# Kernel optimization log

Measured on AMD Instinct MI355X. Metric: run time of the kernel, lower is better.

## Reference

```python
import jax, jax.numpy as jnp
import numpy as np

MARGIN = 0.2
EPS = 1e-6


def setup_inputs() -> dict:
    key = jax.random.key(0)
    k1, k2 = jax.random.split(key)
    B, C = 8192, 1024
    z_label = jax.random.randint(k1, (B,), 0, 256, dtype=jnp.int64 if jax.config.jax_enable_x64 else jnp.int32)
    z_idx = jnp.arange(B, dtype=z_label.dtype)
    z = jax.random.normal(k2, (B, C), dtype=jnp.float32)
    return {"z_label": z_label, "z_idx": z_idx, "z": z}


def reference(z_label, z_idx, z):
    B = z.shape[0]
    k = max(2, int(B * 0.01))  # static: labels overwritten if batch has a single unique label
    all_same = jnp.all(z_label == z_label[0])
    z_label = jnp.where(all_same & (jnp.arange(B) < k), -1, z_label)

    # Vectorized triplet mining (replaces per-sample Python loop):
    # positive: first j with same label, different sample idx; negative: first j with different label.
    label_eq = z_label[:, None] == z_label[None, :]            # [B, B]
    pos_mask = label_eq & (z_idx[:, None] != z_idx[None, :])   # [B, B]
    neg_mask = ~label_eq                                       # [B, B]
    pos_idx = jnp.argmax(pos_mask, axis=1)  # first True (torch.where(...)[0][0])
    neg_idx = jnp.argmax(neg_mask, axis=1)
    valid = pos_mask.any(axis=1) & neg_mask.any(axis=1)        # [B]

    # TripletMarginLoss (p=2, swap=False): d(x,y) = ||x - y + eps||_2
    a, p_emb, n_emb = z, z[pos_idx], z[neg_idx]
    d_ap = jnp.sqrt(jnp.sum((a - p_emb + EPS) ** 2, axis=1))
    d_an = jnp.sqrt(jnp.sum((a - n_emb + EPS) ** 2, axis=1))
    per = jnp.maximum(d_ap - d_an + MARGIN, 0.0)               # [B]

    n_valid = valid.sum()
    vf = valid.astype(per.dtype)
    loss = jnp.where(n_valid > 0,
                     jnp.sum(per * vf) / jnp.maximum(n_valid, 1).astype(per.dtype),
                     jnp.array(0.0, per.dtype))
    return loss
```

## Files before the change

kernel.cpp:

```cpp
#include <hip/hip_runtime.h>

#define MARGIN 0.2f
#define EPSC 1e-6f
#define INF_I 0x7fffffff

__global__ __launch_bounds__(1024) void mine_kernel(
    const int* __restrict__ label, const int* __restrict__ zidx, int B,
    int* __restrict__ g_pos, int* __restrict__ g_neg, int* __restrict__ g_valid)
{
    __shared__ int s_label[8192];
    __shared__ int s_first[258];
    __shared__ int s_second[258];
    __shared__ int s_fd_orig;
    __shared__ int s_fd_eff;
    const int tid = threadIdx.x;
    const int T   = blockDim.x;

    if (tid < 258) { s_first[tid] = INF_I; s_second[tid] = INF_I; }
    if (tid == 0) { s_fd_orig = INF_I; s_fd_eff = INF_I; }
    if ((B & 3) == 0) {
        for (int j = tid * 4; j < B; j += T * 4) {
            int4 v = *(const int4*)(label + j);
            s_label[j] = v.x; s_label[j+1] = v.y; s_label[j+2] = v.z; s_label[j+3] = v.w;
        }
    } else {
        for (int j = tid; j < B; j += T) s_label[j] = label[j];
    }
    __syncthreads();

    const int l0 = s_label[0];
    int lm = INF_I;
    for (int j = tid; j < B; j += T) { if (s_label[j] != l0) { lm = j; break; } }
    if (lm != INF_I) atomicMin(&s_fd_orig, lm);
    __syncthreads();

    const bool all_same = (s_fd_orig == INF_I);
    int k = B / 100; if (k < 2) k = 2;
    if (all_same) { for (int j = tid; j < k && j < B; j += T) s_label[j] = -1; }
    __syncthreads();

    const int l0e = s_label[0];
    lm = INF_I;
    for (int j = tid; j < B; j += T) {
        int l = s_label[j];
        atomicMin(&s_first[l + 1], j);
        if (l != l0e && j < lm) lm = j;
    }
    if (lm != INF_I) atomicMin(&s_fd_eff, lm);
    __syncthreads();

    for (int j = tid; j < B; j += T) {
        int l = s_label[j];
        if (j != s_first[l + 1]) atomicMin(&s_second[l + 1], j);
    }
    __syncthreads();

    const int fd = s_fd_eff;
    for (int i = tid; i < B; i += T) {
        int l  = s_label[i];
        int fo = s_first[l + 1];
        int myidx = zidx[i];
        int pos; bool vp;
        if (zidx[fo] != myidx) { pos = fo; vp = true; }
        else {
            int so = s_second[l + 1];
            if (so != INF_I) { pos = so; vp = true; }
            else             { pos = 0;  vp = false; }
        }
        int neg; bool vn;
        if (l != l0e)        { neg = 0;  vn = true; }
        else if (fd != INF_I){ neg = fd; vn = true; }
        else                 { neg = 0;  vn = false; }
        g_pos[i] = pos; g_neg[i] = neg; g_valid[i] = (vp && vn) ? 1 : 0;
    }
}

__device__ inline void acc8(const float4& av, const float4& pv, const float4& nv,
                            float& sap, float& san) {
    float d;
    d = av.x - pv.x + EPSC; sap += d * d;
    d = av.y - pv.y + EPSC; sap += d * d;
    d = av.z - pv.z + EPSC; sap += d * d;
    d = av.w - pv.w + EPSC; sap += d * d;
    d = av.x - nv.x + EPSC; san += d * d;
    d = av.y - nv.y + EPSC; san += d * d;
    d = av.z - nv.z + EPSC; san += d * d;
    d = av.w - nv.w + EPSC; san += d * d;
}

__global__ __launch_bounds__(256) void dist_kernel(
    const float* __restrict__ z, const int* __restrict__ g_pos,
    const int* __restrict__ g_neg, const int* __restrict__ g_valid,
    int B, int C, float* __restrict__ g_bsum, float* __restrict__ g_bcnt)
{
    const int wave = threadIdx.x >> 6;
    const int lane = threadIdx.x & 63;
    const int i = blockIdx.x * 4 + wave;

    float lsum = 0.f, lcnt = 0.f;
    if (i < B) {
        const float4* a = (const float4*)(z + (size_t)i * C) + lane;
        const float4* p = (const float4*)(z + (size_t)g_pos[i] * C) + lane;
        const float4* n = (const float4*)(z + (size_t)g_neg[i] * C) + lane;
        float sap = 0.f, san = 0.f;
        if (C == 1024) {
            float4 a0 = a[0], a1 = a[64], a2 = a[128], a3 = a[192];
            float4 p0 = p[0], p1 = p[64], p2 = p[128], p3 = p[192];
            float4 n0 = n[0], n1 = n[64], n2 = n[128], n3 = n[192];
            acc8(a0, p0, n0, sap, san);
            acc8(a1, p1, n1, sap, san);
            acc8(a2, p2, n2, sap, san);
            acc8(a3, p3, n3, sap, san);
        } else {
            const int nk = C >> 8;
            for (int k = 0; k < nk; ++k)
                acc8(a[k * 64], p[k * 64], n[k * 64], sap, san);
            for (int c = (nk << 8) + lane; c < C; c += 64) {
                float av = z[(size_t)i * C + c];
                float pv = z[(size_t)g_pos[i] * C + c];
                float nv = z[(size_t)g_neg[i] * C + c];
                float d = av - pv + EPSC; sap += d * d;
                d = av - nv + EPSC; san += d * d;
            }
        }
        for (int off = 32; off; off >>= 1) {
            sap += __shfl_xor(sap, off, 64);
            san += __shfl_xor(san, off, 64);
        }
        if (lane == 0 && g_valid[i]) {
            lsum = fmaxf(sqrtf(sap) - sqrtf(san) + MARGIN, 0.f);
            lcnt = 1.f;
        }
    }

    __shared__ float s_sum[4], s_cnt[4];
    if (lane == 0) { s_sum[wave] = lsum; s_cnt[wave] = lcnt; }
    __syncthreads();
    if (threadIdx.x == 0) {
        float bs = 0.f, bc = 0.f;
        for (int w = 0; w < 4; ++w) { bs += s_sum[w]; bc += s_cnt[w]; }
        g_bsum[blockIdx.x] = bs;
        g_bcnt[blockIdx.x] = bc;
    }
}

__global__ __launch_bounds__(256) void final_kernel(
    const float* __restrict__ g_bsum, const float* __restrict__ g_bcnt,
    int nb, float* __restrict__ out)
{
    const int t = threadIdx.x;
    float s = 0.f, c = 0.f;
    for (int i = t; i < nb; i += blockDim.x) { s += g_bsum[i]; c += g_bcnt[i]; }
    for (int off = 32; off; off >>= 1) {
        s += __shfl_xor(s, off, 64);
        c += __shfl_xor(c, off, 64);
    }
    __shared__ float s_s[4], s_c[4];
    const int wave = t >> 6, lane = t & 63;
    if (lane == 0) { s_s[wave] = s; s_c[wave] = c; }
    __syncthreads();
    if (t == 0) {
        float ts = 0.f, tc = 0.f;
        for (int w = 0; w < 4; ++w) { ts += s_s[w]; tc += s_c[w]; }
        out[0] = (tc > 0.f) ? ts / tc : 0.f;
    }
}

extern "C" void kernel_launch(void* const* d_in, const int* in_sizes, int n_in,
                              void* d_out, int out_size, void* d_ws, size_t ws_size,
                              hipStream_t stream) {
    const int*   z_label = (const int*)d_in[0];
    const int*   z_idx   = (const int*)d_in[1];
    const float* z       = (const float*)d_in[2];
    const int B = in_sizes[0];
    const int C = in_sizes[2] / B;
    float* out = (float*)d_out;

    const int nblk = (B + 3) / 4;

    char* base = (char*)d_ws;
    float* g_bsum = (float*)base;
    float* g_bcnt = g_bsum + nblk;
    int*   g_pos   = (int*)(g_bcnt + nblk);
    int*   g_neg   = g_pos + B;
    int*   g_valid = g_neg + B;

    mine_kernel<<<1, 1024, 0, stream>>>(z_label, z_idx, B, g_pos, g_neg, g_valid);
    dist_kernel<<<nblk, 256, 0, stream>>>(z, g_pos, g_neg, g_valid, B, C,
                                          g_bsum, g_bcnt);
    final_kernel<<<1, 256, 0, stream>>>(g_bsum, g_bcnt, nblk, out);
}
```

Baseline: 97.11 us.

## Fuse triplet mining into distance kernel using per-wave ballot scans

Drops the single-block mining kernel. Each wave now finds its own first positive and first negative by scanning labels 64 at a time with ballots, and the anchor row load is issued before the scan so it overlaps. This removes a serial one-block launch and the round trip through global memory for the pos/neg/valid arrays. In exchange every row repeats a label scan, which is short for random labels but could cost up to O(B) per row for skewed label distributions. It also packs the partial sums as float2 and uses 1024 threads in the final reduction.

```diff
diff --git a/kernel.cpp b/kernel.cpp
--- a/kernel.cpp
+++ b/kernel.cpp
@@ -2,78 +2,6 @@
 
 #define MARGIN 0.2f
 #define EPSC 1e-6f
-#define INF_I 0x7fffffff
-
-__global__ __launch_bounds__(1024) void mine_kernel(
-    const int* __restrict__ label, const int* __restrict__ zidx, int B,
-    int* __restrict__ g_pos, int* __restrict__ g_neg, int* __restrict__ g_valid)
-{
-    __shared__ int s_label[8192];
-    __shared__ int s_first[258];
-    __shared__ int s_second[258];
-    __shared__ int s_fd_orig;
-    __shared__ int s_fd_eff;
-    const int tid = threadIdx.x;
-    const int T   = blockDim.x;
-
-    if (tid < 258) { s_first[tid] = INF_I; s_second[tid] = INF_I; }
-    if (tid == 0) { s_fd_orig = INF_I; s_fd_eff = INF_I; }
-    if ((B & 3) == 0) {
-        for (int j = tid * 4; j < B; j += T * 4) {
-            int4 v = *(const int4*)(label + j);
-            s_label[j] = v.x; s_label[j+1] = v.y; s_label[j+2] = v.z; s_label[j+3] = v.w;
-        }
-    } else {
-        for (int j = tid; j < B; j += T) s_label[j] = label[j];
-    }
-    __syncthreads();
-
-    const int l0 = s_label[0];
-    int lm = INF_I;
-    for (int j = tid; j < B; j += T) { if (s_label[j] != l0) { lm = j; break; } }
-    if (lm != INF_I) atomicMin(&s_fd_orig, lm);
-    __syncthreads();
-
-    const bool all_same = (s_fd_orig == INF_I);
-    int k = B / 100; if (k < 2) k = 2;
-    if (all_same) { for (int j = tid; j < k && j < B; j += T) s_label[j] = -1; }
-    __syncthreads();
-
-    const int l0e = s_label[0];
-    lm = INF_I;
-    for (int j = tid; j < B; j += T) {
-        int l = s_label[j];
-        atomicMin(&s_first[l + 1], j);
-        if (l != l0e && j < lm) lm = j;
-    }
-    if (lm != INF_I) atomicMin(&s_fd_eff, lm);
-    __syncthreads();
-
-    for (int j = tid; j < B; j += T) {
-        int l = s_label[j];
-        if (j != s_first[l + 1]) atomicMin(&s_second[l + 1], j);
-    }
-    __syncthreads();
-
-    const int fd = s_fd_eff;
-    for (int i = tid; i < B; i += T) {
-        int l  = s_label[i];
-        int fo = s_first[l + 1];
-        int myidx = zidx[i];
-        int pos; bool vp;
-        if (zidx[fo] != myidx) { pos = fo; vp = true; }
-        else {
-            int so = s_second[l + 1];
-            if (so != INF_I) { pos = so; vp = true; }
-            else             { pos = 0;  vp = false; }
-        }
-        int neg; bool vn;
-        if (l != l0e)        { neg = 0;  vn = true; }
-        else if (fd != INF_I){ neg = fd; vn = true; }
-        else                 { neg = 0;  vn = false; }
-        g_pos[i] = pos; g_neg[i] = neg; g_valid[i] = (vp && vn) ? 1 : 0;
-    }
-}
 
 __device__ inline void acc8(const float4& av, const float4& pv, const float4& nv,
                             float& sap, float& san) {
@@ -89,9 +17,8 @@
 }
 
 __global__ __launch_bounds__(256) void dist_kernel(
-    const float* __restrict__ z, const int* __restrict__ g_pos,
-    const int* __restrict__ g_neg, const int* __restrict__ g_valid,
-    int B, int C, float* __restrict__ g_bsum, float* __restrict__ g_bcnt)
+    const float* __restrict__ z, const int* __restrict__ label,
+    const int* __restrict__ zidx, int B, int C, float2* __restrict__ g_part)
 {
     const int wave = threadIdx.x >> 6;
     const int lane = threadIdx.x & 63;
@@ -99,12 +26,50 @@
 
     float lsum = 0.f, lcnt = 0.f;
     if (i < B) {
+        const int li    = label[i];
+        const int myidx = zidx[i];
+
         const float4* a = (const float4*)(z + (size_t)i * C) + lane;
-        const float4* p = (const float4*)(z + (size_t)g_pos[i] * C) + lane;
-        const float4* n = (const float4*)(z + (size_t)g_neg[i] * C) + lane;
+        float4 a0, a1, a2, a3;
+        const bool c1024 = (C == 1024);
+        if (c1024) { a0 = a[0]; a1 = a[64]; a2 = a[128]; a3 = a[192]; }
+
+        int pos = -1, neg = -1;
+        for (int j0 = 0; j0 < B && (pos < 0 || neg < 0); j0 += 64) {
+            const int j = j0 + lane;
+            const bool inb = j < B;
+            int lj = 0, xj = 0;
+            if (inb) { lj = label[j]; xj = zidx[j]; }
+            unsigned long long pb = __ballot(inb && lj == li && xj != myidx);
+            unsigned long long nb = __ballot(inb && lj != li);
+            if (pos < 0 && pb) pos = j0 + (__ffsll((unsigned long long)pb) - 1);
+            if (neg < 0 && nb) neg = j0 + (__ffsll((unsigned long long)nb) - 1);
+        }
+        if (neg < 0) {
+            int k = B / 100; if (k < 2) k = 2;
+            const int l0  = li;
+            const int lie = (i < k) ? -1 : l0;
+            pos = -1; neg = -1;
+            for (int j0 = 0; j0 < B && (pos < 0 || neg < 0); j0 += 64) {
+                const int j = j0 + lane;
+                const bool inb = j < B;
+                int xj = 0;
+                if (inb) xj = zidx[j];
+                const int lje = (j < k) ? -1 : l0;
+                unsigned long long pb = __ballot(inb && lje == lie && xj != myidx);
+                unsigned long long nb = __ballot(inb && lje != lie);
+                if (pos < 0 && pb) pos = j0 + (__ffsll((unsigned long long)pb) - 1);
+                if (neg < 0 && nb) neg = j0 + (__ffsll((unsigned long long)nb) - 1);
+            }
+        }
+        const bool valid = (pos >= 0) && (neg >= 0);
+        const int pi = pos < 0 ? 0 : pos;
+        const int ni = neg < 0 ? 0 : neg;
+
+        const float4* p = (const float4*)(z + (size_t)pi * C) + lane;
+        const float4* n = (const float4*)(z + (size_t)ni * C) + lane;
         float sap = 0.f, san = 0.f;
-        if (C == 1024) {
-            float4 a0 = a[0], a1 = a[64], a2 = a[128], a3 = a[192];
+        if (c1024) {
             float4 p0 = p[0], p1 = p[64], p2 = p[128], p3 = p[192];
             float4 n0 = n[0], n1 = n[64], n2 = n[128], n3 = n[192];
             acc8(a0, p0, n0, sap, san);
@@ -113,12 +78,12 @@
             acc8(a3, p3, n3, sap, san);
         } else {
             const int nk = C >> 8;
-            for (int k = 0; k < nk; ++k)
-                acc8(a[k * 64], p[k * 64], n[k * 64], sap, san);
+            for (int kk = 0; kk < nk; ++kk)
+                acc8(a[kk * 64], p[kk * 64], n[kk * 64], sap, san);
             for (int c = (nk << 8) + lane; c < C; c += 64) {
                 float av = z[(size_t)i * C + c];
-                float pv = z[(size_t)g_pos[i] * C + c];
-                float nv = z[(size_t)g_neg[i] * C + c];
+                float pv = z[(size_t)pi * C + c];
+                float nv = z[(size_t)ni * C + c];
                 float d = av - pv + EPSC; sap += d * d;
                 d = av - nv + EPSC; san += d * d;
             }
@@ -127,7 +92,7 @@
             sap += __shfl_xor(sap, off, 64);
             san += __shfl_xor(san, off, 64);
         }
-        if (lane == 0 && g_valid[i]) {
+        if (lane == 0 && valid) {
             lsum = fmaxf(sqrtf(sap) - sqrtf(san) + MARGIN, 0.f);
             lcnt = 1.f;
         }
@@ -139,29 +104,31 @@
     if (threadIdx.x == 0) {
         float bs = 0.f, bc = 0.f;
         for (int w = 0; w < 4; ++w) { bs += s_sum[w]; bc += s_cnt[w]; }
-        g_bsum[blockIdx.x] = bs;
-        g_bcnt[blockIdx.x] = bc;
+        g_part[blockIdx.x] = make_float2(bs, bc);
     }
 }
 
-__global__ __launch_bounds__(256) void final_kernel(
-    const float* __restrict__ g_bsum, const float* __restrict__ g_bcnt,
-    int nb, float* __restrict__ out)
+__global__ __launch_bounds__(1024) void final_kernel(
+    const float2* __restrict__ g_part, int nb, float* __restrict__ out)
 {
     const int t = threadIdx.x;
     float s = 0.f, c = 0.f;
-    for (int i = t; i < nb; i += blockDim.x) { s += g_bsum[i]; c += g_bcnt[i]; }
+    for (int idx = t; idx < nb; idx += blockDim.x) {
+        float2 v = g_part[idx];
+        s += v.x; c += v.y;
+    }
     for (int off = 32; off; off >>= 1) {
         s += __shfl_xor(s, off, 64);
         c += __shfl_xor(c, off, 64);
     }
-    __shared__ float s_s[4], s_c[4];
+    __shared__ float s_s[16], s_c[16];
     const int wave = t >> 6, lane = t & 63;
     if (lane == 0) { s_s[wave] = s; s_c[wave] = c; }
     __syncthreads();
     if (t == 0) {
         float ts = 0.f, tc = 0.f;
-        for (int w = 0; w < 4; ++w) { ts += s_s[w]; tc += s_c[w]; }
+        const int nw = blockDim.x >> 6;
+        for (int w = 0; w < nw; ++w) { ts += s_s[w]; tc += s_c[w]; }
         out[0] = (tc > 0.f) ? ts / tc : 0.f;
     }
 }
@@ -177,16 +144,8 @@
     float* out = (float*)d_out;
 
     const int nblk = (B + 3) / 4;
+    float2* g_part = (float2*)d_ws;
 
-    char* base = (char*)d_ws;
-    float* g_bsum = (float*)base;
-    float* g_bcnt = g_bsum + nblk;
-    int*   g_pos   = (int*)(g_bcnt + nblk);
-    int*   g_neg   = g_pos + B;
-    int*   g_valid = g_neg + B;
-
-    mine_kernel<<<1, 1024, 0, stream>>>(z_label, z_idx, B, g_pos, g_neg, g_valid);
-    dist_kernel<<<nblk, 256, 0, stream>>>(z, g_pos, g_neg, g_valid, B, C,
-                                          g_bsum, g_bcnt);
-    final_kernel<<<1, 256, 0, stream>>>(g_bsum, g_bcnt, nblk, out);
+    dist_kernel<<<nblk, 256, 0, stream>>>(z, z_label, z_idx, B, C, g_part);
+    final_kernel<<<1, 1024, 0, stream>>>(g_part, nblk, out);
 }
```

After: 89.35 us. 8.0% less time.
